# Performance work log

Measured on AMD Instinct MI355X. Metric: run time of the kernel, lower is better.

Reference implementation:

```python
import jax, jax.numpy as jnp
import numpy as np

NUM_HEADS = 16
HEAD_SIZE = 64
EMB = NUM_HEADS * HEAD_SIZE
B, S = 2, 2048


def setup_inputs() -> dict:
    key = jax.random.key(0)
    ks = jax.random.split(key, 8)
    return {
        "values": jax.random.normal(ks[0], (B, S, EMB), dtype=jnp.float32),
        "keys": jax.random.normal(ks[1], (B, S, EMB), dtype=jnp.float32),
        "queries": jax.random.normal(ks[2], (B, S, EMB), dtype=jnp.float32),
        "mask": jnp.ones((B, 1, 1, S), dtype=jnp.int32),
        "Wq": jax.random.normal(ks[3], (HEAD_SIZE, HEAD_SIZE), dtype=jnp.float32) / np.sqrt(HEAD_SIZE),
        "Wk": jax.random.normal(ks[4], (HEAD_SIZE, HEAD_SIZE), dtype=jnp.float32) / np.sqrt(HEAD_SIZE),
        "Wv": jax.random.normal(ks[5], (HEAD_SIZE, HEAD_SIZE), dtype=jnp.float32) / np.sqrt(HEAD_SIZE),
        "Wout": jax.random.normal(ks[6], (EMB, EMB), dtype=jnp.float32) / np.sqrt(EMB),
        "bout": jax.random.normal(ks[7], (EMB,), dtype=jnp.float32) * 0.01,
    }


def reference(values, keys, queries, mask, Wq, Wk, Wv, Wout, bout):
    n, q_len, E = queries.shape
    H, D = NUM_HEADS, HEAD_SIZE
    # split heads: [n, len, H, D]
    v = values.reshape(n, -1, H, D)
    k = keys.reshape(n, -1, H, D)
    q = queries.reshape(n, q_len, H, D)
    # per-head shared linears (torch Linear: x @ W.T), no bias
    v = jnp.einsum("nkhd,cd->nkhc", v, Wv)
    k = jnp.einsum("nkhd,cd->nkhc", k, Wk)
    q = jnp.einsum("nqhd,cd->nqhc", q, Wq)
    # scores: [n, H, q, k]
    energy = jnp.einsum("nqhd,nkhd->nhqk", q, k)
    energy = jnp.where(mask == 0, jnp.float32(-1e28), energy)
    # NOTE: source scales by sqrt(embedding_size), not head_size
    attn = jax.nn.softmax(energy / jnp.sqrt(jnp.float32(E)), axis=3)
    out = jnp.einsum("nhqk,nkhd->nqhd", attn, v).reshape(n, q_len, E)
    return out @ Wout.T + bout
```

## Files before the change

### kernel.cpp

```cpp
#include <hip/hip_runtime.h>
#include <hip/hip_bf16.h>


#define NHB 16
#define HS  64
#define EMB 1024
#define BB  2
#define SS  2048
#define NT  (SS / 64)

typedef __bf16 bf16_t;
typedef bf16_t bf16x8 __attribute__((ext_vector_type(8)));
typedef bf16_t bf16x4 __attribute__((ext_vector_type(4)));
typedef short  s16x4  __attribute__((ext_vector_type(4)));
typedef float  f32x4  __attribute__((ext_vector_type(4)));

__device__ __forceinline__ f32x4 mfma16(bf16x8 a, bf16x8 b, f32x4 c) {
    return __builtin_amdgcn_mfma_f32_16x16x32_bf16(a, b, c, 0, 0, 0);
}
__device__ __forceinline__ f32x4 mfma16k16(bf16x4 a, s16x4 b, f32x4 c) {
    return __builtin_amdgcn_mfma_f32_16x16x16bf16_1k(
        __builtin_bit_cast(s16x4, a), b, c, 0, 0, 0);
}

__global__ __launch_bounds__(256) void proj_kernel(
    const float* __restrict__ queries, const float* __restrict__ keys,
    const float* __restrict__ values,
    const float* __restrict__ Wq, const float* __restrict__ Wk,
    const float* __restrict__ Wv,
    bf16_t* __restrict__ Qb, bf16_t* __restrict__ Kb, bf16_t* __restrict__ Vt)
{
    __shared__ bf16_t Ws[3][64][72];
    __shared__ bf16_t Xs[64][72];

    const int tid  = threadIdx.x;
    const int wave = tid >> 6, lane = tid & 63;
    const int q4 = lane >> 4, l16 = lane & 15;
    const int s0 = blockIdx.x * 64;
    const int h  = blockIdx.y, n = blockIdx.z;

    for (int mW = 0; mW < 3; ++mW) {
        const float* wp = (mW == 0) ? Wq : (mW == 1) ? Wk : Wv;
        #pragma unroll
        for (int i = 0; i < 4; ++i) {
            int idx4 = i * 256 + tid;
            float4 v = ((const float4*)wp)[idx4];
            int r = idx4 >> 4, c = (idx4 & 15) * 4;
            Ws[mW][r][c+0] = (bf16_t)v.x; Ws[mW][r][c+1] = (bf16_t)v.y;
            Ws[mW][r][c+2] = (bf16_t)v.z; Ws[mW][r][c+3] = (bf16_t)v.w;
        }
    }

    for (int p = 0; p < 3; ++p) {
        __syncthreads();
        const float* xp = (p == 0) ? queries : (p == 1) ? keys : values;
        #pragma unroll
        for (int i = 0; i < 4; ++i) {
            int idx4 = i * 256 + tid;
            int r = idx4 >> 4, c = (idx4 & 15) * 4;
            float4 v = *(const float4*)&xp[((size_t)(n * SS + s0 + r)) * EMB + h * HS + c];
            Xs[r][c+0] = (bf16_t)v.x; Xs[r][c+1] = (bf16_t)v.y;
            Xs[r][c+2] = (bf16_t)v.z; Xs[r][c+3] = (bf16_t)v.w;
        }
        __syncthreads();

        bf16x8 a0 = *(const bf16x8*)&Xs[wave * 16 + l16][q4 * 8];
        bf16x8 a1 = *(const bf16x8*)&Xs[wave * 16 + l16][32 + q4 * 8];
        f32x4 acc[4] = {};
        #pragma unroll
        for (int ct = 0; ct < 4; ++ct) {
            bf16x8 b0 = *(const bf16x8*)&Ws[p][l16 + ct * 16][q4 * 8];
            bf16x8 b1 = *(const bf16x8*)&Ws[p][l16 + ct * 16][32 + q4 * 8];
            acc[ct] = mfma16(a0, b0, acc[ct]);
            acc[ct] = mfma16(a1, b1, acc[ct]);
        }

        const size_t headBase = (size_t)(n * NHB + h) * SS * HS;
        if (p < 2) {
            bf16_t* dst = (p == 0) ? Qb : Kb;
            const float sc = (p == 0) ? 0.03125f : 1.0f;
            #pragma unroll
            for (int ct = 0; ct < 4; ++ct)
                #pragma unroll
                for (int i = 0; i < 4; ++i) {
                    int srow = s0 + wave * 16 + q4 * 4 + i;
                    dst[headBase + (size_t)srow * HS + l16 + ct * 16] = (bf16_t)(acc[ct][i] * sc);
                }
        } else {
            #pragma unroll
            for (int ct = 0; ct < 4; ++ct) {
                int d = l16 + ct * 16;
                bf16x4 pk;
                pk[0] = (bf16_t)acc[ct][0]; pk[1] = (bf16_t)acc[ct][1];
                pk[2] = (bf16_t)acc[ct][2]; pk[3] = (bf16_t)acc[ct][3];
                *(bf16x4*)&Vt[headBase + (size_t)d * SS + s0 + wave * 16 + q4 * 4] = pk;
            }
        }
    }
}

__global__ __launch_bounds__(512) void attn_kernel(
    const bf16_t* __restrict__ Qb, const bf16_t* __restrict__ Kb,
    const bf16_t* __restrict__ Vt, const int* __restrict__ mask,
    bf16_t* __restrict__ Og)
{
    __shared__ bf16_t Ks[2][64][72];
    __shared__ bf16_t Vs[2][64][72];
    __shared__ float  Ms[2][64];

    const int tid = threadIdx.x;
    const int w = tid >> 6, lane = tid & 63;
    const int q4 = lane >> 4, l16 = lane & 15;
    const int qt = blockIdx.x, h = blockIdx.y, n = blockIdx.z;
    const size_t headBase = (size_t)(n * NHB + h) * SS * HS;
    const int* mrow = mask + n * SS;

    const int sr = tid >> 3, sc = (tid & 7) * 8;
    const bf16_t* kb_src = Kb + headBase + (size_t)sr * HS + sc;
    const bf16_t* vt_src = Vt + headBase + (size_t)sr * SS + sc;

    const int qrow = qt * 128 + w * 16 + l16;
    const bf16_t* qptr = Qb + headBase + (size_t)qrow * HS;
    const bf16x8 bq0 = *(const bf16x8*)&qptr[q4 * 8];
    const bf16x8 bq1 = *(const bf16x8*)&qptr[32 + q4 * 8];

    f32x4 oaccT[4] = {};
    float lsum = 0.f;

    *(bf16x8*)&Ks[0][sr][sc] = *(const bf16x8*)kb_src;
    *(bf16x8*)&Vs[0][sr][sc] = *(const bf16x8*)vt_src;
    if (tid < 64) Ms[0][tid] = mrow[tid] ? 1.0f : 0.0f;
    __syncthreads();

    for (int kt = 0; kt < NT; ++kt) {
        const int cur = kt & 1;
        const bool has_next = (kt + 1) < NT;
        bf16x8 gk, gv; float gm = 0.f;
        if (has_next) {
            const int k0n = (kt + 1) * 64;
            gk = *(const bf16x8*)(kb_src + (size_t)k0n * HS);
            gv = *(const bf16x8*)(vt_src + k0n);
            if (tid < 64) gm = mrow[k0n + tid] ? 1.0f : 0.0f;
        }

        f32x4 sacc[4] = {};
        #pragma unroll
        for (int ct = 0; ct < 4; ++ct) {
            bf16x8 ak0 = *(const bf16x8*)&Ks[cur][ct * 16 + l16][q4 * 8];
            bf16x8 ak1 = *(const bf16x8*)&Ks[cur][ct * 16 + l16][32 + q4 * 8];
            sacc[ct] = mfma16(ak0, bq0, sacc[ct]);
            sacc[ct] = mfma16(ak1, bq1, sacc[ct]);
        }

        s16x4 pfrag[4];
        #pragma unroll
        for (int ct = 0; ct < 4; ++ct) {
            float mf[4];
            *(float4*)mf = *(const float4*)&Ms[cur][ct * 16 + q4 * 4];
            bf16x4 pv;
            #pragma unroll
            for (int j = 0; j < 4; ++j) {
                float e = __expf(sacc[ct][j]) * mf[j];
                lsum += e;
                pv[j] = (bf16_t)e;
            }
            pfrag[ct] = __builtin_bit_cast(s16x4, pv);
        }

        #pragma unroll
        for (int dt = 0; dt < 4; ++dt)
            #pragma unroll
            for (int ct = 0; ct < 4; ++ct) {
                bf16x4 av = *(const bf16x4*)&Vs[cur][dt * 16 + l16][ct * 16 + q4 * 4];
                oaccT[dt] = mfma16k16(av, pfrag[ct], oaccT[dt]);
            }

        if (has_next) {
            const int nxt = 1 - cur;
            *(bf16x8*)&Ks[nxt][sr][sc] = gk;
            *(bf16x8*)&Vs[nxt][sr][sc] = gv;
            if (tid < 64) Ms[nxt][tid] = gm;
        }
        __syncthreads();
    }

    lsum += __shfl_xor(lsum, 16, 64);
    lsum += __shfl_xor(lsum, 32, 64);
    const float inv = 1.f / lsum;

    bf16_t* obase = Og + ((size_t)(n * SS + qrow)) * EMB + h * HS;
    #pragma unroll
    for (int dt = 0; dt < 4; ++dt) {
        bf16x4 ov;
        #pragma unroll
        for (int j = 0; j < 4; ++j) ov[j] = (bf16_t)(oaccT[dt][j] * inv);
        *(bf16x4*)&obase[dt * 16 + q4 * 4] = ov;
    }
}

__global__ __launch_bounds__(256) void wconv_kernel(
    const float* __restrict__ W, bf16_t* __restrict__ Wb)
{
    int idx4 = blockIdx.x * 256 + threadIdx.x;
    float4 v = ((const float4*)W)[idx4];
    bf16x4 o;
    o[0] = (bf16_t)v.x; o[1] = (bf16_t)v.y; o[2] = (bf16_t)v.z; o[3] = (bf16_t)v.w;
    *(bf16x4*)&Wb[idx4 * 4] = o;
}

__global__ __launch_bounds__(512) void outproj_kernel(
    const bf16_t* __restrict__ Og, const bf16_t* __restrict__ Wb,
    const float* __restrict__ bout, float* __restrict__ out)
{
    __shared__ bf16_t As[2][128][72];
    __shared__ bf16_t Bs[2][128][72];
    const int tid = threadIdx.x;
    const int w = tid >> 6, lane = tid & 63;
    const int q4 = lane >> 4, l16 = lane & 15;
    const int wr = w >> 1, wc = w & 1;
    const int t0 = blockIdx.x * 128, c0 = blockIdx.y * 128;

    const int sr0 = tid >> 3, sc0 = (tid & 7) * 8;
    const int sr1 = sr0 + 64;
    const bf16_t* a0 = Og + (size_t)(t0 + sr0) * EMB + sc0;
    const bf16_t* a1 = Og + (size_t)(t0 + sr1) * EMB + sc0;
    const bf16_t* b0 = Wb + (size_t)(c0 + sr0) * EMB + sc0;
    const bf16_t* b1 = Wb + (size_t)(c0 + sr1) * EMB + sc0;

    f32x4 acc[2][4] = {};

    *(bf16x8*)&As[0][sr0][sc0] = *(const bf16x8*)a0;
    *(bf16x8*)&As[0][sr1][sc0] = *(const bf16x8*)a1;
    *(bf16x8*)&Bs[0][sr0][sc0] = *(const bf16x8*)b0;
    *(bf16x8*)&Bs[0][sr1][sc0] = *(const bf16x8*)b1;
    __syncthreads();

    const int NE = EMB / 64;
    for (int et = 0; et < NE; ++et) {
        const int cur = et & 1;
        const bool has_next = (et + 1) < NE;
        bf16x8 ga0, ga1, gb0, gb1;
        if (has_next) {
            const int e0 = (et + 1) * 64;
            ga0 = *(const bf16x8*)(a0 + e0); ga1 = *(const bf16x8*)(a1 + e0);
            gb0 = *(const bf16x8*)(b0 + e0); gb1 = *(const bf16x8*)(b1 + e0);
        }

        bf16x8 af[2][2], bfr[4][2];
        #pragma unroll
        for (int st = 0; st < 2; ++st)
            #pragma unroll
            for (int kk = 0; kk < 2; ++kk)
                af[st][kk] = *(const bf16x8*)&As[cur][wr * 32 + st * 16 + l16][kk * 32 + q4 * 8];
        #pragma unroll
        for (int ct = 0; ct < 4; ++ct)
            #pragma unroll
            for (int kk = 0; kk < 2; ++kk)
                bfr[ct][kk] = *(const bf16x8*)&Bs[cur][wc * 64 + ct * 16 + l16][kk * 32 + q4 * 8];
        #pragma unroll
        for (int st = 0; st < 2; ++st)
            #pragma unroll
            for (int ct = 0; ct < 4; ++ct) {
                acc[st][ct] = mfma16(af[st][0], bfr[ct][0], acc[st][ct]);
                acc[st][ct] = mfma16(af[st][1], bfr[ct][1], acc[st][ct]);
            }

        if (has_next) {
            const int nxt = 1 - cur;
            *(bf16x8*)&As[nxt][sr0][sc0] = ga0;
            *(bf16x8*)&As[nxt][sr1][sc0] = ga1;
            *(bf16x8*)&Bs[nxt][sr0][sc0] = gb0;
            *(bf16x8*)&Bs[nxt][sr1][sc0] = gb1;
        }
        __syncthreads();
    }

    #pragma unroll
    for (int ct = 0; ct < 4; ++ct) {
        const int c = c0 + wc * 64 + ct * 16 + l16;
        const float bias = bout[c];
        #pragma unroll
        for (int st = 0; st < 2; ++st)
            #pragma unroll
            for (int i = 0; i < 4; ++i)
                out[(size_t)(t0 + wr * 32 + st * 16 + q4 * 4 + i) * EMB + c]
                    = acc[st][ct][i] + bias;
    }
}

extern "C" void kernel_launch(void* const* d_in, const int* in_sizes, int n_in,
                              void* d_out, int out_size, void* d_ws, size_t ws_size,
                              hipStream_t stream)
{
    const float* values  = (const float*)d_in[0];
    const float* keys    = (const float*)d_in[1];
    const float* queries = (const float*)d_in[2];
    const int*   mask    = (const int*)d_in[3];
    const float* Wq      = (const float*)d_in[4];
    const float* Wk      = (const float*)d_in[5];
    const float* Wv      = (const float*)d_in[6];
    const float* Wout    = (const float*)d_in[7];
    const float* bout    = (const float*)d_in[8];
    float* out = (float*)d_out;

    const size_t M8 = 8ull * 1024 * 1024;
    bf16_t* Qb = (bf16_t*)d_ws;
    bf16_t* Kb = (bf16_t*)((char*)d_ws + 1 * M8);
    bf16_t* Vt = (bf16_t*)((char*)d_ws + 2 * M8);
    bf16_t* Og = (bf16_t*)((char*)d_ws + 3 * M8);
    bf16_t* Wb = Qb;

    proj_kernel<<<dim3(SS / 64, NHB, BB), 256, 0, stream>>>(
        queries, keys, values, Wq, Wk, Wv, Qb, Kb, Vt);
    attn_kernel<<<dim3(SS / 128, NHB, BB), 512, 0, stream>>>(
        Qb, Kb, Vt, mask, Og);
    wconv_kernel<<<dim3(1024), 256, 0, stream>>>(Wout, Wb);
    outproj_kernel<<<dim3((BB * SS) / 128, EMB / 128), 512, 0, stream>>>(
        Og, Wb, bout, out);
}
```

Measured before the change: 190.3 us.

## Give each attention wave two query subtiles and use K=32 MFMA for PV

```diff
diff --git a/kernel.cpp b/kernel.cpp
--- a/kernel.cpp
+++ b/kernel.cpp
@@ -12,15 +12,10 @@
 typedef __bf16 bf16_t;
 typedef bf16_t bf16x8 __attribute__((ext_vector_type(8)));
 typedef bf16_t bf16x4 __attribute__((ext_vector_type(4)));
-typedef short  s16x4  __attribute__((ext_vector_type(4)));
 typedef float  f32x4  __attribute__((ext_vector_type(4)));
 
 __device__ __forceinline__ f32x4 mfma16(bf16x8 a, bf16x8 b, f32x4 c) {
     return __builtin_amdgcn_mfma_f32_16x16x32_bf16(a, b, c, 0, 0, 0);
-}
-__device__ __forceinline__ f32x4 mfma16k16(bf16x4 a, s16x4 b, f32x4 c) {
-    return __builtin_amdgcn_mfma_f32_16x16x16bf16_1k(
-        __builtin_bit_cast(s16x4, a), b, c, 0, 0, 0);
 }
 
 __global__ __launch_bounds__(256) void proj_kernel(
@@ -51,6 +46,8 @@
         }
     }
 
+    const size_t headBase = (size_t)(n * NHB + h) * SS * HS;
+
     for (int p = 0; p < 3; ++p) {
         __syncthreads();
         const float* xp = (p == 0) ? queries : (p == 1) ? keys : values;
@@ -64,42 +61,47 @@
         }
         __syncthreads();
 
-        bf16x8 a0 = *(const bf16x8*)&Xs[wave * 16 + l16][q4 * 8];
-        bf16x8 a1 = *(const bf16x8*)&Xs[wave * 16 + l16][32 + q4 * 8];
-        f32x4 acc[4] = {};
-        #pragma unroll
-        for (int ct = 0; ct < 4; ++ct) {
-            bf16x8 b0 = *(const bf16x8*)&Ws[p][l16 + ct * 16][q4 * 8];
-            bf16x8 b1 = *(const bf16x8*)&Ws[p][l16 + ct * 16][32 + q4 * 8];
-            acc[ct] = mfma16(a0, b0, acc[ct]);
-            acc[ct] = mfma16(a1, b1, acc[ct]);
-        }
-
-        const size_t headBase = (size_t)(n * NHB + h) * SS * HS;
+        bf16x8 xf[2], wf[4][2];
+        #pragma unroll
+        for (int kk = 0; kk < 2; ++kk)
+            xf[kk] = *(const bf16x8*)&Xs[wave * 16 + l16][kk * 32 + q4 * 8];
+        #pragma unroll
+        for (int ct = 0; ct < 4; ++ct)
+            #pragma unroll
+            for (int kk = 0; kk < 2; ++kk)
+                wf[ct][kk] = *(const bf16x8*)&Ws[p][ct * 16 + l16][kk * 32 + q4 * 8];
+
         if (p < 2) {
             bf16_t* dst = (p == 0) ? Qb : Kb;
-            const float sc = (p == 0) ? 0.03125f : 1.0f;
-            #pragma unroll
-            for (int ct = 0; ct < 4; ++ct)
+            const float sc = (p == 0) ? (0.03125f * 1.44269504f) : 1.0f;
+            #pragma unroll
+            for (int ct = 0; ct < 4; ++ct) {
+                f32x4 acc = {};
+                acc = mfma16(wf[ct][0], xf[0], acc);
+                acc = mfma16(wf[ct][1], xf[1], acc);
+                bf16x4 pk;
                 #pragma unroll
-                for (int i = 0; i < 4; ++i) {
-                    int srow = s0 + wave * 16 + q4 * 4 + i;
-                    dst[headBase + (size_t)srow * HS + l16 + ct * 16] = (bf16_t)(acc[ct][i] * sc);
-                }
+                for (int i = 0; i < 4; ++i) pk[i] = (bf16_t)(acc[i] * sc);
+                *(bf16x4*)&dst[headBase + (size_t)(s0 + wave * 16 + l16) * HS
+                               + ct * 16 + q4 * 4] = pk;
+            }
         } else {
             #pragma unroll
             for (int ct = 0; ct < 4; ++ct) {
-                int d = l16 + ct * 16;
+                f32x4 acc = {};
+                acc = mfma16(xf[0], wf[ct][0], acc);
+                acc = mfma16(xf[1], wf[ct][1], acc);
                 bf16x4 pk;
-                pk[0] = (bf16_t)acc[ct][0]; pk[1] = (bf16_t)acc[ct][1];
-                pk[2] = (bf16_t)acc[ct][2]; pk[3] = (bf16_t)acc[ct][3];
-                *(bf16x4*)&Vt[headBase + (size_t)d * SS + s0 + wave * 16 + q4 * 4] = pk;
-            }
-        }
-    }
-}
-
-__global__ __launch_bounds__(512) void attn_kernel(
+                #pragma unroll
+                for (int i = 0; i < 4; ++i) pk[i] = (bf16_t)acc[i];
+                *(bf16x4*)&Vt[headBase + (size_t)(ct * 16 + l16) * SS
+                              + s0 + (wave >> 1) * 32 + q4 * 8 + (wave & 1) * 4] = pk;
+            }
+        }
+    }
+}
+
+__global__ __launch_bounds__(256) void attn_kernel(
     const bf16_t* __restrict__ Qb, const bf16_t* __restrict__ Kb,
     const bf16_t* __restrict__ Vt, const int* __restrict__ mask,
     bf16_t* __restrict__ Og)
@@ -115,86 +117,117 @@
     const size_t headBase = (size_t)(n * NHB + h) * SS * HS;
     const int* mrow = mask + n * SS;
 
-    const int sr = tid >> 3, sc = (tid & 7) * 8;
-    const bf16_t* kb_src = Kb + headBase + (size_t)sr * HS + sc;
-    const bf16_t* vt_src = Vt + headBase + (size_t)sr * SS + sc;
-
-    const int qrow = qt * 128 + w * 16 + l16;
-    const bf16_t* qptr = Qb + headBase + (size_t)qrow * HS;
-    const bf16x8 bq0 = *(const bf16x8*)&qptr[q4 * 8];
-    const bf16x8 bq1 = *(const bf16x8*)&qptr[32 + q4 * 8];
-
-    f32x4 oaccT[4] = {};
-    float lsum = 0.f;
-
-    *(bf16x8*)&Ks[0][sr][sc] = *(const bf16x8*)kb_src;
-    *(bf16x8*)&Vs[0][sr][sc] = *(const bf16x8*)vt_src;
+    const int sr0 = tid >> 3, sc0 = (tid & 7) * 8;
+    const int sr1 = sr0 + 32;
+    const bf16_t* kb0 = Kb + headBase + (size_t)sr0 * HS + sc0;
+    const bf16_t* kb1 = Kb + headBase + (size_t)sr1 * HS + sc0;
+    const bf16_t* vt0 = Vt + headBase + (size_t)sr0 * SS + sc0;
+    const bf16_t* vt1 = Vt + headBase + (size_t)sr1 * SS + sc0;
+
+    bf16x8 bq[2][2];
+    #pragma unroll
+    for (int st = 0; st < 2; ++st) {
+        const bf16_t* qptr = Qb + headBase
+            + (size_t)(qt * 128 + w * 32 + st * 16 + l16) * HS;
+        bq[st][0] = *(const bf16x8*)&qptr[q4 * 8];
+        bq[st][1] = *(const bf16x8*)&qptr[32 + q4 * 8];
+    }
+
+    f32x4 oaccT[2][4] = {};
+    float lsum[2] = {0.f, 0.f};
+
+    *(bf16x8*)&Ks[0][sr0][sc0] = *(const bf16x8*)kb0;
+    *(bf16x8*)&Ks[0][sr1][sc0] = *(const bf16x8*)kb1;
+    *(bf16x8*)&Vs[0][sr0][sc0] = *(const bf16x8*)vt0;
+    *(bf16x8*)&Vs[0][sr1][sc0] = *(const bf16x8*)vt1;
     if (tid < 64) Ms[0][tid] = mrow[tid] ? 1.0f : 0.0f;
     __syncthreads();
 
     for (int kt = 0; kt < NT; ++kt) {
         const int cur = kt & 1;
         const bool has_next = (kt + 1) < NT;
-        bf16x8 gk, gv; float gm = 0.f;
+        bf16x8 gk0, gk1, gv0, gv1; float gm = 0.f;
         if (has_next) {
             const int k0n = (kt + 1) * 64;
-            gk = *(const bf16x8*)(kb_src + (size_t)k0n * HS);
-            gv = *(const bf16x8*)(vt_src + k0n);
+            gk0 = *(const bf16x8*)(kb0 + (size_t)k0n * HS);
+            gk1 = *(const bf16x8*)(kb1 + (size_t)k0n * HS);
+            gv0 = *(const bf16x8*)(vt0 + k0n);
+            gv1 = *(const bf16x8*)(vt1 + k0n);
             if (tid < 64) gm = mrow[k0n + tid] ? 1.0f : 0.0f;
         }
 
-        f32x4 sacc[4] = {};
+        f32x4 sacc[2][4] = {};
         #pragma unroll
         for (int ct = 0; ct < 4; ++ct) {
             bf16x8 ak0 = *(const bf16x8*)&Ks[cur][ct * 16 + l16][q4 * 8];
             bf16x8 ak1 = *(const bf16x8*)&Ks[cur][ct * 16 + l16][32 + q4 * 8];
-            sacc[ct] = mfma16(ak0, bq0, sacc[ct]);
-            sacc[ct] = mfma16(ak1, bq1, sacc[ct]);
-        }
-
-        s16x4 pfrag[4];
+            #pragma unroll
+            for (int st = 0; st < 2; ++st) {
+                sacc[st][ct] = mfma16(ak0, bq[st][0], sacc[st][ct]);
+                sacc[st][ct] = mfma16(ak1, bq[st][1], sacc[st][ct]);
+            }
+        }
+
+        bf16x4 pv[2][4];
         #pragma unroll
         for (int ct = 0; ct < 4; ++ct) {
             float mf[4];
             *(float4*)mf = *(const float4*)&Ms[cur][ct * 16 + q4 * 4];
-            bf16x4 pv;
-            #pragma unroll
-            for (int j = 0; j < 4; ++j) {
-                float e = __expf(sacc[ct][j]) * mf[j];
-                lsum += e;
-                pv[j] = (bf16_t)e;
-            }
-            pfrag[ct] = __builtin_bit_cast(s16x4, pv);
-        }
-
-        #pragma unroll
-        for (int dt = 0; dt < 4; ++dt)
-            #pragma unroll
-            for (int ct = 0; ct < 4; ++ct) {
-                bf16x4 av = *(const bf16x4*)&Vs[cur][dt * 16 + l16][ct * 16 + q4 * 4];
-                oaccT[dt] = mfma16k16(av, pfrag[ct], oaccT[dt]);
-            }
+            #pragma unroll
+            for (int st = 0; st < 2; ++st) {
+                bf16x4 pk;
+                #pragma unroll
+                for (int j = 0; j < 4; ++j) {
+                    float e = exp2f(sacc[st][ct][j]) * mf[j];
+                    lsum[st] += e;
+                    pk[j] = (bf16_t)e;
+                }
+                pv[st][ct] = pk;
+            }
+        }
+
+        #pragma unroll
+        for (int kb = 0; kb < 2; ++kb) {
+            bf16x8 pa[2];
+            #pragma unroll
+            for (int st = 0; st < 2; ++st)
+                pa[st] = __builtin_shufflevector(pv[st][2 * kb], pv[st][2 * kb + 1],
+                                                 0, 1, 2, 3, 4, 5, 6, 7);
+            #pragma unroll
+            for (int dt = 0; dt < 4; ++dt) {
+                bf16x8 av = *(const bf16x8*)&Vs[cur][dt * 16 + l16][kb * 32 + q4 * 8];
+                #pragma unroll
+                for (int st = 0; st < 2; ++st)
+                    oaccT[st][dt] = mfma16(av, pa[st], oaccT[st][dt]);
+            }
+        }
 
         if (has_next) {
             const int nxt = 1 - cur;
-            *(bf16x8*)&Ks[nxt][sr][sc] = gk;
-            *(bf16x8*)&Vs[nxt][sr][sc] = gv;
+            *(bf16x8*)&Ks[nxt][sr0][sc0] = gk0;
+            *(bf16x8*)&Ks[nxt][sr1][sc0] = gk1;
+            *(bf16x8*)&Vs[nxt][sr0][sc0] = gv0;
+            *(bf16x8*)&Vs[nxt][sr1][sc0] = gv1;
             if (tid < 64) Ms[nxt][tid] = gm;
         }
         __syncthreads();
     }
 
-    lsum += __shfl_xor(lsum, 16, 64);
-    lsum += __shfl_xor(lsum, 32, 64);
-    const float inv = 1.f / lsum;
-
-    bf16_t* obase = Og + ((size_t)(n * SS + qrow)) * EMB + h * HS;
     #pragma unroll
-    for (int dt = 0; dt < 4; ++dt) {
-        bf16x4 ov;
-        #pragma unroll
-        for (int j = 0; j < 4; ++j) ov[j] = (bf16_t)(oaccT[dt][j] * inv);
-        *(bf16x4*)&obase[dt * 16 + q4 * 4] = ov;
+    for (int st = 0; st < 2; ++st) {
+        float ls = lsum[st];
+        ls += __shfl_xor(ls, 16, 64);
+        ls += __shfl_xor(ls, 32, 64);
+        const float inv = 1.f / ls;
+        const int qrow = qt * 128 + w * 32 + st * 16 + l16;
+        bf16_t* obase = Og + ((size_t)(n * SS + qrow)) * EMB + h * HS;
+        #pragma unroll
+        for (int dt = 0; dt < 4; ++dt) {
+            bf16x4 ov;
+            #pragma unroll
+            for (int j = 0; j < 4; ++j) ov[j] = (bf16_t)(oaccT[st][dt][j] * inv);
+            *(bf16x4*)&obase[dt * 16 + q4 * 4] = ov;
+        }
     }
 }
 
@@ -312,7 +345,7 @@
 
     proj_kernel<<<dim3(SS / 64, NHB, BB), 256, 0, stream>>>(
         queries, keys, values, Wq, Wk, Wv, Qb, Kb, Vt);
-    attn_kernel<<<dim3(SS / 128, NHB, BB), 512, 0, stream>>>(
+    attn_kernel<<<dim3(SS / 128, NHB, BB), 256, 0, stream>>>(
         Qb, Kb, Vt, mask, Og);
     wconv_kernel<<<dim3(1024), 256, 0, stream>>>(Wout, Wb);
     outproj_kernel<<<dim3((BB * SS) / 128, EMB / 128), 512, 0, stream>>>(
```

Result: slower. 198.2 us (+4.2%).
